# Kernel tuning notes

Hardware: AMD Instinct MI355X
Metric: run time of the kernel (lower is better)

Reference implementation:

```python
import jax, jax.numpy as jnp
import numpy as np

D_MODEL = 768
N_LAYER = 2
VOCAB = 32000
D_STATE = 16
D_INNER = 1536
DT_RANK = 48
D_CONV = 4
B, L = 2, 1024
EPS = 1e-5


def rmsnorm(x, w):
    return x * jax.lax.rsqrt(jnp.mean(x * x, axis=-1, keepdims=True) + EPS) * w


def selective_scan(u, dt, A, Bm, Cm, Dv):
    # u: (b,l,d)  dt: (b,l,d)  A: (d,n)  Bm,Cm: (b,l,n)  Dv: (d,)
    dA = jnp.einsum('bld,dn->bldn', dt, A)
    dB_u = jnp.einsum('bld,bld,bln->bldn', dt, u, Bm)
    # shift dA left by one step along l, zero-pad at end, reverse-cumsum, exp
    t = jnp.concatenate([dA[:, 1:], jnp.zeros_like(dA[:, :1])], axis=1)
    dA_cumsum = jnp.exp(jnp.flip(jnp.cumsum(jnp.flip(t, axis=1), axis=1), axis=1))
    x = dB_u * dA_cumsum
    x = jnp.cumsum(x, axis=1) / (dA_cumsum + 1e-12)
    y = jnp.einsum('bldn,bln->bld', x, Cm)
    return y + u * Dv


def mamba_block(x, W_in, conv_w, conv_b, x_proj_w, dt_proj_w, dt_proj_b, A_log, D_param, W_out):
    b, l, d = x.shape
    xz = x @ W_in.T                       # (b,l,2*d_inner)
    xs, res = xz[..., :D_INNER], xz[..., D_INNER:]
    # depthwise causal conv1d: left-pad d_conv-1 -> output length l
    xt = jnp.transpose(xs, (0, 2, 1))     # (b,d_in,l)
    xt = jax.lax.conv_general_dilated(
        xt, conv_w, window_strides=(1,), padding=[(D_CONV - 1, 0)],
        dimension_numbers=('NCH', 'OIH', 'NCH'), feature_group_count=D_INNER)
    xt = xt + conv_b[None, :, None]
    xs = jax.nn.silu(jnp.transpose(xt, (0, 2, 1)))
    # SSM
    A = -jnp.exp(A_log.astype(jnp.float32))
    x_dbl = xs @ x_proj_w.T               # (b,l,dt_rank+2n)
    delta = x_dbl[..., :DT_RANK]
    Bm = x_dbl[..., DT_RANK:DT_RANK + D_STATE]
    Cm = x_dbl[..., DT_RANK + D_STATE:]
    delta = jax.nn.softplus(delta @ dt_proj_w.T + dt_proj_b)
    y = selective_scan(xs, delta, A, Bm, Cm, D_param.astype(jnp.float32))
    y = y * jax.nn.silu(res)
    return y @ W_out.T


def setup_inputs() -> dict:
    key = jax.random.key(0)
    ks = jax.random.split(key, 12)
    s = 0.02
    inp = {
        'input_ids': jax.random.randint(ks[0], (B, L), 0, VOCAB),
        'embedding': jax.random.normal(ks[1], (VOCAB, D_MODEL), jnp.float32) * s,
        'W_in': jax.random.normal(ks[2], (N_LAYER, 2 * D_INNER, D_MODEL), jnp.float32) * s,
        'conv_w': jax.random.normal(ks[3], (N_LAYER, D_INNER, 1, D_CONV), jnp.float32) * 0.2,
        'conv_b': jnp.zeros((N_LAYER, D_INNER), jnp.float32),
        'x_proj_w': jax.random.normal(ks[4], (N_LAYER, DT_RANK + 2 * D_STATE, D_INNER), jnp.float32) * s,
        'dt_proj_w': jax.random.normal(ks[5], (N_LAYER, D_INNER, DT_RANK), jnp.float32) * s,
        'dt_proj_b': jnp.full((N_LAYER, D_INNER), -4.0, jnp.float32),
        'A_log': jnp.broadcast_to(jnp.log(jnp.arange(1, D_STATE + 1, dtype=jnp.float32)), (N_LAYER, D_INNER, D_STATE)) * jnp.ones((N_LAYER, D_INNER, 1), jnp.float32),
        'D_param': jnp.ones((N_LAYER, D_INNER), jnp.float32),
        'W_out': jax.random.normal(ks[6], (N_LAYER, D_MODEL, D_INNER), jnp.float32) * s,
        'norm_w': jnp.ones((N_LAYER, D_MODEL), jnp.float32),
        'norm_f_w': jnp.ones((D_MODEL,), jnp.float32),
    }
    return inp


def reference(input_ids, embedding, W_in, conv_w, conv_b, x_proj_w, dt_proj_w,
              dt_proj_b, A_log, D_param, W_out, norm_w, norm_f_w):
    x = embedding[input_ids]              # (b,l,d_model)
    for i in range(N_LAYER):
        x = mamba_block(rmsnorm(x, norm_w[i]), W_in[i], conv_w[i], conv_b[i],
                        x_proj_w[i], dt_proj_w[i], dt_proj_b[i], A_log[i],
                        D_param[i], W_out[i]) + x
    x = rmsnorm(x, norm_f_w)
    return x @ embedding.T                # tied lm_head -> (b,l,vocab)
```

## Files before the change

### kernel.cpp

```cpp
#include <hip/hip_runtime.h>
#include <math.h>

#define DM    768
#define DS    16
#define DI    1536
#define DTR   48
#define NB    2
#define NL    1024
#define NBL   (NB*NL)
#define NVOC  32000
#define XDL   128

typedef __attribute__((ext_vector_type(8))) short bf16x8;
typedef __attribute__((ext_vector_type(4))) float floatx4;

static __device__ __forceinline__ float siluf(float x){ return x / (1.0f + expf(-x)); }
static __device__ __forceinline__ float softplusf(float x){ return (x > 20.0f) ? x : log1pf(expf(x)); }
static __device__ __forceinline__ unsigned short f2bf(float f){
    unsigned int u = __float_as_uint(f);
    u += 0x7FFFu + ((u >> 16) & 1u);
    return (unsigned short)(u >> 16);
}

#define GLL16(g, l) __builtin_amdgcn_global_load_lds( \
    (const __attribute__((address_space(1))) unsigned int*)(g), \
    (__attribute__((address_space(3))) unsigned int*)(l), 16, 0, 0)

__global__ __launch_bounds__(256) void cast_bf16_kernel(const float* __restrict__ in,
        unsigned short* __restrict__ out, int n4){
    int i = blockIdx.x*256 + threadIdx.x;
    if (i >= n4) return;
    float4 v = ((const float4*)in)[i];
    ushort4 o = { f2bf(v.x), f2bf(v.y), f2bf(v.z), f2bf(v.w) };
    ((ushort4*)out)[i] = o;
}

__global__ __launch_bounds__(256) void cast_pad_xproj_kernel(const float* __restrict__ in,
        unsigned short* __restrict__ out){
    int q = blockIdx.x*256 + threadIdx.x;
    const int QL = 128*1536/4;
    if (q >= 2*QL) return;
    int layer = q / QL, rem = q - layer*QL;
    int row = rem / (1536/4), c4 = rem - row*(1536/4);
    ushort4 o = {0,0,0,0};
    if (row < 80){
        float4 v = ((const float4*)(in + ((size_t)layer*80 + row)*1536))[c4];
        o.x = f2bf(v.x); o.y = f2bf(v.y); o.z = f2bf(v.z); o.w = f2bf(v.w);
    }
    ((ushort4*)out)[q] = o;
}

__global__ __launch_bounds__(256) void zero_f32_kernel(float* __restrict__ p, int n4){
    int i = blockIdx.x*256 + threadIdx.x;
    if (i >= n4) return;
    float4 z = {0.f,0.f,0.f,0.f};
    ((float4*)p)[i] = z;
}

__global__ __launch_bounds__(256) void embed_kernel(const int* __restrict__ ids,
        const float* __restrict__ emb, float* __restrict__ x){
    int i = blockIdx.x*256 + threadIdx.x;
    if (i >= NBL*DM) return;
    int row = i / DM, c = i - row*DM;
    x[i] = emb[(size_t)ids[row]*DM + c];
}

__global__ __launch_bounds__(256) void rmsnorm_bf16_kernel(const float* __restrict__ x,
        const float* __restrict__ w, unsigned short* __restrict__ h){
    int row = blockIdx.x;
    const float* xr = x + (size_t)row*DM;
    __shared__ float red[256];
    float s = 0.f;
    for (int c = threadIdx.x; c < DM; c += 256){ float v = xr[c]; s += v*v; }
    red[threadIdx.x] = s; __syncthreads();
    for (int o = 128; o > 0; o >>= 1){
        if (threadIdx.x < o) red[threadIdx.x] += red[threadIdx.x + o];
        __syncthreads();
    }
    float r = 1.0f / sqrtf(red[0]*(1.0f/DM) + 1e-5f);
    for (int c = threadIdx.x; c < DM; c += 256) h[(size_t)row*DM + c] = f2bf(xr[c]*r*w[c]);
}

template<int MODE>
__global__ __launch_bounds__(256) void mfma_gemm_nt(const unsigned short* __restrict__ A,
        const unsigned short* __restrict__ B, float* __restrict__ C,
        int M, int N, int K, int Kc){
    __shared__ __align__(16) unsigned short Asm[128*64];
    __shared__ __align__(16) unsigned short Bsm[128*64];
    int tid = threadIdx.x;

    int nwg  = gridDim.x * gridDim.y;
    int orig = blockIdx.y * gridDim.x + blockIdx.x;
    int q = nwg >> 3, r = nwg & 7;
    int xcd = orig & 7;
    int wg  = (xcd < r ? xcd*(q+1) : r*(q+1) + (xcd-r)*q) + (orig >> 3);
    int mb  = wg % gridDim.y;
    int nb  = wg / gridDim.y;
    int m0 = mb * 128, n0 = nb * 128;

    int lane = tid & 63;
    int quad = lane >> 4, l16 = lane & 15;
    int wave = tid >> 6;
    int wm = (wave >> 1) * 64, wn = (wave & 1) * 64;

    floatx4 acc[4][4] = {};

    int srow = tid >> 3;
    int csrc = ((tid & 7) ^ ((tid >> 3) & 7)) * 8;
    const unsigned short* Ag = A + (size_t)(m0 + srow) * K + csrc;
    const unsigned short* Bg = B + (size_t)(n0 + srow) * K + csrc;

    int k0 = blockIdx.z * Kc;
    for (int kt = k0; kt < k0 + Kc; kt += 64){
        #pragma unroll
        for (int qr = 0; qr < 4; qr++){
            GLL16(Ag + (size_t)qr*32*K + kt, &Asm[((size_t)qr*256 + tid)*8]);
            GLL16(Bg + (size_t)qr*32*K + kt, &Bsm[((size_t)qr*256 + tid)*8]);
        }
        __syncthreads();

        #pragma unroll
        for (int ks = 0; ks < 2; ks++){
            bf16x8 af[4], bff[4];
            #pragma unroll
            for (int i = 0; i < 4; i++){
                int ar = wm + i*16 + l16;
                af[i]  = *(const bf16x8*)&Asm[ar*64 + ((ks*4 + quad) ^ (ar & 7))*8];
                int br = wn + i*16 + l16;
                bff[i] = *(const bf16x8*)&Bsm[br*64 + ((ks*4 + quad) ^ (br & 7))*8];
            }
            #pragma unroll
            for (int i = 0; i < 4; i++)
                #pragma unroll
                for (int j = 0; j < 4; j++)
                    acc[i][j] = __builtin_amdgcn_mfma_f32_16x16x32_bf16(af[i], bff[j], acc[i][j], 0, 0, 0);
        }
        __syncthreads();
    }

    #pragma unroll
    for (int i = 0; i < 4; i++){
        int gm = m0 + wm + i*16 + quad*4;
        #pragma unroll
        for (int j = 0; j < 4; j++){
            int gn = n0 + wn + j*16 + l16;
            float* cp = C + (size_t)gm*N + gn;
            #pragma unroll
            for (int rr = 0; rr < 4; rr++){
                float v = acc[i][j][rr];
                if (MODE == 2){
                    atomicAdd(&cp[(size_t)rr*N], v);
                } else {
                    if (MODE == 1) v += cp[(size_t)rr*N];
                    cp[(size_t)rr*N] = v;
                }
            }
        }
    }
}

__global__ __launch_bounds__(256) void gemm_nt(const float* __restrict__ A,
        const float* __restrict__ Bw, float* __restrict__ C, const float* __restrict__ bias,
        int M, int N, int K, int lda, int ldb, int ldc, int act, int accum){
    __shared__ float As[16][68];
    __shared__ float Bs[16][68];
    int tid = threadIdx.x;
    int tn = tid & 15, tm = tid >> 4;
    int n0 = blockIdx.x * 64, m0 = blockIdx.y * 64;
    float acc[4][4] = {{0.f}};
    for (int kt = 0; kt < K; kt += 16){
        int gk = kt + tn;
        bool kok = gk < K;
        #pragma unroll
        for (int r = 0; r < 4; r++){
            int m = tm + r*16;
            As[tn][m] = (kok && (m0 + m) < M) ? A[(size_t)(m0+m)*lda + gk] : 0.f;
            Bs[tn][m] = (kok && (n0 + m) < N) ? Bw[(size_t)(n0+m)*ldb + gk] : 0.f;
        }
        __syncthreads();
        #pragma unroll
        for (int kk = 0; kk < 16; kk++){
            float a0 = As[kk][tm*4+0], a1 = As[kk][tm*4+1], a2 = As[kk][tm*4+2], a3 = As[kk][tm*4+3];
            float b0 = Bs[kk][tn*4+0], b1 = Bs[kk][tn*4+1], b2 = Bs[kk][tn*4+2], b3 = Bs[kk][tn*4+3];
            acc[0][0] += a0*b0; acc[0][1] += a0*b1; acc[0][2] += a0*b2; acc[0][3] += a0*b3;
            acc[1][0] += a1*b0; acc[1][1] += a1*b1; acc[1][2] += a1*b2; acc[1][3] += a1*b3;
            acc[2][0] += a2*b0; acc[2][1] += a2*b1; acc[2][2] += a2*b2; acc[2][3] += a2*b3;
            acc[3][0] += a3*b0; acc[3][1] += a3*b1; acc[3][2] += a3*b2; acc[3][3] += a3*b3;
        }
        __syncthreads();
    }
    #pragma unroll
    for (int i = 0; i < 4; i++){
        int gm = m0 + tm*4 + i;
        if (gm >= M) continue;
        #pragma unroll
        for (int j = 0; j < 4; j++){
            int gn = n0 + tn*4 + j;
            if (gn >= N) continue;
            float v = acc[i][j];
            if (bias) v += bias[gn];
            if (act == 1) v = softplusf(v);
            size_t ci = (size_t)gm*ldc + gn;
            if (accum) v += C[ci];
            C[ci] = v;
        }
    }
}

__global__ __launch_bounds__(256) void conv_silu_kernel(const float* __restrict__ xz,
        const float* __restrict__ cw, const float* __restrict__ cb,
        float* __restrict__ xs, unsigned short* __restrict__ xs_bf){
    int i = blockIdx.x*256 + threadIdx.x;
    if (i >= NBL*DI) return;
    int bl = i / DI, d = i - bl*DI;
    int l = bl & (NL-1);
    float acc = cb[d];
    #pragma unroll
    for (int j = 0; j < 4; j++){
        int off = j - 3;
        if (l + off >= 0) acc += cw[d*4+j] * xz[(size_t)(bl + off)*(2*DI) + d];
    }
    float v = siluf(acc);
    xs[i] = v;
    xs_bf[i] = f2bf(v);
}

__global__ __launch_bounds__(256) void transpose_kernel(const float* __restrict__ in,
        float* __restrict__ out, int R, int Ccols, int ldin){
    __shared__ float tile[32][33];
    int c0 = blockIdx.x*32, r0 = blockIdx.y*32;
    int tx = threadIdx.x & 31, ty = threadIdx.x >> 5;
    #pragma unroll
    for (int i = 0; i < 32; i += 8){
        int r = r0 + ty + i, c = c0 + tx;
        tile[ty+i][tx] = (r < R && c < Ccols) ? in[(size_t)r*ldin + c] : 0.f;
    }
    __syncthreads();
    #pragma unroll
    for (int i = 0; i < 32; i += 8){
        int r = r0 + tx, c = c0 + ty + i;
        if (c < Ccols && r < R) out[(size_t)c*R + r] = tile[tx][ty+i];
    }
}

__global__ __launch_bounds__(256) void transpose2_kernel(const float* __restrict__ in1,
        float* __restrict__ out1, const float* __restrict__ in2, float* __restrict__ out2){
    __shared__ float tile[32][33];
    int c0 = blockIdx.x*32, r0 = blockIdx.y*32;
    int tx = threadIdx.x & 31, ty = threadIdx.x >> 5;
    #pragma unroll
    for (int i = 0; i < 32; i += 8)
        tile[ty+i][tx] = in1[(size_t)(r0+ty+i)*DI + (c0+tx)];
    __syncthreads();
    #pragma unroll
    for (int i = 0; i < 32; i += 8)
        out1[(size_t)(c0+ty+i)*NBL + (r0+tx)] = tile[tx][ty+i];
    __syncthreads();
    #pragma unroll
    for (int i = 0; i < 32; i += 8)
        tile[ty+i][tx] = in2[(size_t)(r0+ty+i)*DI + (c0+tx)];
    __syncthreads();
    #pragma unroll
    for (int i = 0; i < 32; i += 8)
        out2[(size_t)(c0+ty+i)*NBL + (r0+tx)] = tile[tx][ty+i];
}

static __device__ __forceinline__ float wave_incl_scan(float v, int lane){
    #pragma unroll
    for (int s = 1; s < 64; s <<= 1){
        float t = __shfl_up(v, s, 64);
        if (lane >= s) v += t;
    }
    return v;
}

__global__ __launch_bounds__(256) void scan_kernel(const float* __restrict__ u_t,
        const float* dt_t, const float* __restrict__ xdbl_t,
        const float* __restrict__ A_log, const float* __restrict__ Dp,
        float* y_t){
    int tid = threadIdx.x, lane = tid & 63, w = tid >> 6;
    int bd = blockIdx.x*4 + w;
    int b = bd / DI, d = bd - b*DI;
    size_t rowoff = (size_t)d*NBL + b*NL;
    int l0 = lane*16;

    float d16[16], u16[16];
    #pragma unroll
    for (int q = 0; q < 4; q++){
        float4 v = ((const float4*)(dt_t + rowoff + l0))[q];
        d16[q*4+0]=v.x; d16[q*4+1]=v.y; d16[q*4+2]=v.z; d16[q*4+3]=v.w;
        float4 u = ((const float4*)(u_t + rowoff + l0))[q];
        u16[q*4+0]=u.x; u16[q*4+1]=u.y; u16[q*4+2]=u.z; u16[q*4+3]=u.w;
    }
    float pl[16], yac[16];
    float run = 0.f;
    #pragma unroll
    for (int r = 0; r < 16; r++){ run += d16[r]; pl[r] = run; yac[r] = 0.f; }
    float inc = wave_incl_scan(run, lane);
    float ex  = inc - run;
    float T   = __shfl(inc, 63, 64);
    #pragma unroll
    for (int r = 0; r < 16; r++) pl[r] += ex;

    for (int n = 0; n < DS; n++){
        float An = -expf(A_log[d*DS + n]);
        float Bv[16], Cv[16];
        #pragma unroll
        for (int q = 0; q < 4; q++){
            float4 bv = ((const float4*)(xdbl_t + (size_t)(DTR+n)*NBL + b*NL + l0))[q];
            Bv[q*4+0]=bv.x; Bv[q*4+1]=bv.y; Bv[q*4+2]=bv.z; Bv[q*4+3]=bv.w;
            float4 cv = ((const float4*)(xdbl_t + (size_t)(DTR+DS+n)*NBL + b*NL + l0))[q];
            Cv[q*4+0]=cv.x; Cv[q*4+1]=cv.y; Cv[q*4+2]=cv.z; Cv[q*4+3]=cv.w;
        }
        float e[16], zl[16];
        float zrun = 0.f;
        #pragma unroll
        for (int r = 0; r < 16; r++){
            e[r] = expf(An * (T - pl[r]));
            zrun += d16[r]*u16[r]*Bv[r]*e[r];
            zl[r] = zrun;
        }
        float zinc = wave_incl_scan(zrun, lane);
        float zex  = zinc - zrun;
        #pragma unroll
        for (int r = 0; r < 16; r++){
            float num = zex + zl[r];
            yac[r] += num / (e[r] + 1e-12f) * Cv[r];
        }
    }
    float Dv = Dp[d];
    #pragma unroll
    for (int q = 0; q < 4; q++){
        float4 yo;
        yo.x = yac[q*4+0] + u16[q*4+0]*Dv;
        yo.y = yac[q*4+1] + u16[q*4+1]*Dv;
        yo.z = yac[q*4+2] + u16[q*4+2]*Dv;
        yo.w = yac[q*4+3] + u16[q*4+3]*Dv;
        ((float4*)(y_t + rowoff + l0))[q] = yo;
    }
}

__global__ __launch_bounds__(256) void gate_transpose_kernel(const float* __restrict__ y_t,
        const float* __restrict__ xz, unsigned short* __restrict__ ys){
    __shared__ float tile[32][33];
    int c0 = blockIdx.x*32;
    int r0 = blockIdx.y*32;
    int tx = threadIdx.x & 31, ty = threadIdx.x >> 5;
    #pragma unroll
    for (int i = 0; i < 32; i += 8)
        tile[ty+i][tx] = y_t[(size_t)(r0+ty+i)*NBL + (c0+tx)];
    __syncthreads();
    #pragma unroll
    for (int i = 0; i < 32; i += 8){
        int d  = r0 + tx;
        int bl = c0 + ty + i;
        float g = siluf(xz[(size_t)bl*(2*DI) + DI + d]);
        ys[(size_t)bl*DI + d] = f2bf(tile[tx][ty+i] * g);
    }
}

extern "C" void kernel_launch(void* const* d_in, const int* in_sizes, int n_in,
                              void* d_out, int out_size, void* d_ws, size_t ws_size,
                              hipStream_t stream){
    const int*   ids    = (const int*)d_in[0];
    const float* emb    = (const float*)d_in[1];
    const float* W_in   = (const float*)d_in[2];
    const float* convw  = (const float*)d_in[3];
    const float* convb  = (const float*)d_in[4];
    const float* xproj  = (const float*)d_in[5];
    const float* dtw    = (const float*)d_in[6];
    const float* dtbias = (const float*)d_in[7];
    const float* Alog   = (const float*)d_in[8];
    const float* Dpar   = (const float*)d_in[9];
    const float* Wout   = (const float*)d_in[10];
    const float* normw  = (const float*)d_in[11];
    const float* normf  = (const float*)d_in[12];
    float* out = (float*)d_out;

    float* ws    = (float*)d_ws;
    float* x     = ws;
    float* xz    = x     + (size_t)NBL*DM;
    float* xs    = xz    + (size_t)NBL*2*DI;
    float* xdbl  = xs    + (size_t)NBL*DI;
    float* xdblt = xdbl  + (size_t)NBL*XDL;
    float* dtb   = xdblt + (size_t)NBL*80;
    float* dtt   = dtb   + (size_t)NBL*DI;
    float* ut    = dtt   + (size_t)NBL*DI;
    unsigned short* h_bf   = (unsigned short*)(ut + (size_t)NBL*DI);
    unsigned short* emb_bf = h_bf    + (size_t)NBL*DM;
    unsigned short* win_bf = emb_bf  + (size_t)NVOC*DM;
    unsigned short* wout_bf= win_bf  + (size_t)2*2*DI*DM;
    unsigned short* xs_bf  = wout_bf + (size_t)2*DM*DI;
    unsigned short* xprojp = xs_bf   + (size_t)NBL*DI;
    unsigned short* ys_bf  = (unsigned short*)dtb;
    float* yt = dtt;

    cast_bf16_kernel<<<(NVOC*DM/4 + 255)/256, 256, 0, stream>>>(emb, emb_bf, NVOC*DM/4);
    cast_bf16_kernel<<<(2*2*DI*DM/4 + 255)/256, 256, 0, stream>>>(W_in, win_bf, 2*2*DI*DM/4);
    cast_bf16_kernel<<<(2*DM*DI/4 + 255)/256, 256, 0, stream>>>(Wout, wout_bf, 2*DM*DI/4);
    cast_pad_xproj_kernel<<<(2*128*1536/4 + 255)/256, 256, 0, stream>>>(xproj, xprojp);

    embed_kernel<<<(NBL*DM + 255)/256, 256, 0, stream>>>(ids, emb, x);

    for (int i = 0; i < 2; i++){
        rmsnorm_bf16_kernel<<<NBL, 256, 0, stream>>>(x, normw + i*DM, h_bf);
        mfma_gemm_nt<0><<<dim3(3072/128, NBL/128, 1), 256, 0, stream>>>(
                h_bf, win_bf + (size_t)i*2*DI*DM, xz, NBL, 2*DI, DM, DM);
        conv_silu_kernel<<<(NBL*DI + 255)/256, 256, 0, stream>>>(xz, convw + i*DI*4, convb + i*DI, xs, xs_bf);
        zero_f32_kernel<<<(NBL*XDL/4 + 255)/256, 256, 0, stream>>>(xdbl, NBL*XDL/4);
        mfma_gemm_nt<2><<<dim3(1, NBL/128, 8), 256, 0, stream>>>(
                xs_bf, xprojp + (size_t)i*128*DI, xdbl, NBL, XDL, DI, DI/8);
        gemm_nt<<<dim3(24,32), 256, 0, stream>>>(xdbl, dtw + (size_t)i*DI*DTR, dtb, dtbias + i*DI,
                NBL, DI, DTR, XDL, DTR, DI, 1, 0);
        transpose_kernel<<<dim3(3,64),  256, 0, stream>>>(xdbl, xdblt, NBL, 80, XDL);
        transpose2_kernel<<<dim3(48,64), 256, 0, stream>>>(dtb, dtt, xs, ut);
        scan_kernel<<<NB*DI/4, 256, 0, stream>>>(ut, dtt, xdblt,
                Alog + (size_t)i*DI*DS, Dpar + i*DI, yt);
        gate_transpose_kernel<<<dim3(64,48), 256, 0, stream>>>(yt, xz, ys_bf);
        mfma_gemm_nt<2><<<dim3(DM/128, NBL/128, 2), 256, 0, stream>>>(
                ys_bf, wout_bf + (size_t)i*DM*DI, x, NBL, DM, DI, DI/2);
    }

    rmsnorm_bf16_kernel<<<NBL, 256, 0, stream>>>(x, normf, h_bf);
    mfma_gemm_nt<0><<<dim3(NVOC/128, NBL/128, 1), 256, 0, stream>>>(
            h_bf, emb_bf, out, NBL, NVOC, DM, DM);
}
```

Before: 888.8 us.

## Double-buffer GEMM LDS tiles and use wave-shuffle reduction in RMSNorm

The MFMA GEMM now holds two LDS buffers per operand and issues the global-to-LDS loads for the next K-step before computing on the current one. This lets memory latency overlap with MFMA work and drops one barrier per iteration. LDS use doubles to 64KB per block, which may lower occupancy. RMSNorm also replaces its shared-memory tree reduction with wavefront xor-shuffles plus a 4-entry cross-wave sum, cutting barriers.

After: 877.6 us. About the same (-1.3%).

```diff
diff --git a/kernel.cpp b/kernel.cpp
--- a/kernel.cpp
+++ b/kernel.cpp
@@ -69,24 +69,25 @@
         const float* __restrict__ w, unsigned short* __restrict__ h){
     int row = blockIdx.x;
     const float* xr = x + (size_t)row*DM;
-    __shared__ float red[256];
+    __shared__ float red[4];
+    int tid = threadIdx.x, lane = tid & 63, wv = tid >> 6;
     float s = 0.f;
-    for (int c = threadIdx.x; c < DM; c += 256){ float v = xr[c]; s += v*v; }
-    red[threadIdx.x] = s; __syncthreads();
-    for (int o = 128; o > 0; o >>= 1){
-        if (threadIdx.x < o) red[threadIdx.x] += red[threadIdx.x + o];
-        __syncthreads();
-    }
-    float r = 1.0f / sqrtf(red[0]*(1.0f/DM) + 1e-5f);
-    for (int c = threadIdx.x; c < DM; c += 256) h[(size_t)row*DM + c] = f2bf(xr[c]*r*w[c]);
+    for (int c = tid; c < DM; c += 256){ float v = xr[c]; s += v*v; }
+    #pragma unroll
+    for (int o = 32; o > 0; o >>= 1) s += __shfl_xor(s, o, 64);
+    if (lane == 0) red[wv] = s;
+    __syncthreads();
+    float tot = red[0] + red[1] + red[2] + red[3];
+    float r = 1.0f / sqrtf(tot*(1.0f/DM) + 1e-5f);
+    for (int c = tid; c < DM; c += 256) h[(size_t)row*DM + c] = f2bf(xr[c]*r*w[c]);
 }
 
 template<int MODE>
 __global__ __launch_bounds__(256) void mfma_gemm_nt(const unsigned short* __restrict__ A,
         const unsigned short* __restrict__ B, float* __restrict__ C,
         int M, int N, int K, int Kc){
-    __shared__ __align__(16) unsigned short Asm[128*64];
-    __shared__ __align__(16) unsigned short Bsm[128*64];
+    __shared__ __align__(16) unsigned short Asm[2][128*64];
+    __shared__ __align__(16) unsigned short Bsm[2][128*64];
     int tid = threadIdx.x;
 
     int nwg  = gridDim.x * gridDim.y;
@@ -111,13 +112,25 @@
     const unsigned short* Bg = B + (size_t)(n0 + srow) * K + csrc;
 
     int k0 = blockIdx.z * Kc;
-    for (int kt = k0; kt < k0 + Kc; kt += 64){
-        #pragma unroll
-        for (int qr = 0; qr < 4; qr++){
-            GLL16(Ag + (size_t)qr*32*K + kt, &Asm[((size_t)qr*256 + tid)*8]);
-            GLL16(Bg + (size_t)qr*32*K + kt, &Bsm[((size_t)qr*256 + tid)*8]);
-        }
-        __syncthreads();
+    int nsteps = Kc >> 6;
+
+    #pragma unroll
+    for (int qr = 0; qr < 4; qr++){
+        GLL16(Ag + (size_t)qr*32*K + k0, &Asm[0][(qr*256 + tid)*8]);
+        GLL16(Bg + (size_t)qr*32*K + k0, &Bsm[0][(qr*256 + tid)*8]);
+    }
+    __syncthreads();
+
+    int cur = 0;
+    for (int s = 0; s < nsteps; s++){
+        if (s + 1 < nsteps){
+            int kt = k0 + (s+1)*64;
+            #pragma unroll
+            for (int qr = 0; qr < 4; qr++){
+                GLL16(Ag + (size_t)qr*32*K + kt, &Asm[cur^1][(qr*256 + tid)*8]);
+                GLL16(Bg + (size_t)qr*32*K + kt, &Bsm[cur^1][(qr*256 + tid)*8]);
+            }
+        }
 
         #pragma unroll
         for (int ks = 0; ks < 2; ks++){
@@ -125,9 +138,9 @@
             #pragma unroll
             for (int i = 0; i < 4; i++){
                 int ar = wm + i*16 + l16;
-                af[i]  = *(const bf16x8*)&Asm[ar*64 + ((ks*4 + quad) ^ (ar & 7))*8];
+                af[i]  = *(const bf16x8*)&Asm[cur][ar*64 + ((ks*4 + quad) ^ (ar & 7))*8];
                 int br = wn + i*16 + l16;
-                bff[i] = *(const bf16x8*)&Bsm[br*64 + ((ks*4 + quad) ^ (br & 7))*8];
+                bff[i] = *(const bf16x8*)&Bsm[cur][br*64 + ((ks*4 + quad) ^ (br & 7))*8];
             }
             #pragma unroll
             for (int i = 0; i < 4; i++)
@@ -136,6 +149,7 @@
                     acc[i][j] = __builtin_amdgcn_mfma_f32_16x16x32_bf16(af[i], bff[j], acc[i][j], 0, 0, 0);
         }
         __syncthreads();
+        cur ^= 1;
     }
 
     #pragma unroll
```
